# Performance work log

Hardware: AMD Instinct MI355X
Metric: run time of the kernel (lower is better)

## Reference

```python
import jax, jax.numpy as jnp
import numpy as np

E, H, V = 512, 1024, 50257
B, S = 64, 2048

def setup_inputs() -> dict:
    key = jax.random.key(0)
    ks = jax.random.split(key, 11)
    s_e, s_h, s_c, s_o = E ** -0.5, H ** -0.5, (2 * H) ** -0.5, H ** -0.5
    return {
        "input_seq_embedded": jax.random.normal(ks[0], (1, B, E), jnp.float32),
        "last_hidden": jax.random.normal(ks[1], (1, B, H), jnp.float32),
        "encoder_outputs": jax.random.normal(ks[2], (S, B, H), jnp.float32),
        # PyTorch GRU params (gate order: r, z, n)
        "w_ih": jax.random.uniform(ks[3], (3 * H, E), jnp.float32, -s_h, s_h),
        "w_hh": jax.random.uniform(ks[4], (3 * H, H), jnp.float32, -s_h, s_h),
        "b_ih": jax.random.uniform(ks[5], (3 * H,), jnp.float32, -s_h, s_h),
        "b_hh": jax.random.uniform(ks[6], (3 * H,), jnp.float32, -s_h, s_h),
        "W_concat": jax.random.uniform(ks[7], (H, 2 * H), jnp.float32, -s_c, s_c),
        "b_concat": jax.random.uniform(ks[8], (H,), jnp.float32, -s_c, s_c),
        "W_out": jax.random.uniform(ks[9], (V, H), jnp.float32, -s_o, s_o),
        "b_out": jax.random.uniform(ks[10], (V,), jnp.float32, -s_o, s_o),
    }

def reference(input_seq_embedded, last_hidden, encoder_outputs,
              w_ih, w_hh, b_ih, b_hh, W_concat, b_concat, W_out, b_out):
    x = input_seq_embedded[0]          # [B, E]
    h = last_hidden[0]                 # [B, H]
    # GRU cell (PyTorch semantics, gates r,z,n)
    gi = x @ w_ih.T + b_ih             # [B, 3H]
    gh = h @ w_hh.T + b_hh             # [B, 3H]
    gi_r, gi_z, gi_n = jnp.split(gi, 3, axis=1)
    gh_r, gh_z, gh_n = jnp.split(gh, 3, axis=1)
    r = jax.nn.sigmoid(gi_r + gh_r)
    z = jax.nn.sigmoid(gi_z + gh_z)
    n = jnp.tanh(gi_n + r * gh_n)
    h_new = (1.0 - z) * n + z * h      # [B, H]
    hidden = h_new[None]               # [1, B, H]
    rnn_output = h_new                 # [B, H] (seq dim squeezed)
    # 'dot' attention: energy[b,s] = <rnn_output[b], encoder_outputs[s,b]>
    energies = jnp.einsum('bh,sbh->bs', rnn_output, encoder_outputs)  # [B, S]
    attn_weights = jax.nn.softmax(energies, axis=1)                   # [B, S]
    context = jnp.einsum('bs,sbh->bh', attn_weights, encoder_outputs) # [B, H]
    concat_input = jnp.concatenate([rnn_output, context], axis=1)     # [B, 2H]
    concat_output = jnp.tanh(concat_input @ W_concat.T + b_concat)    # [B, H]
    output = concat_output @ W_out.T + b_out                          # [B, V]
    return output, hidden, attn_weights[:, None, :]
```

## Files before the change

### kernel.cpp

```cpp
#include <hip/hip_runtime.h>
#include <hip/hip_bf16.h>

#define E_DIM 512
#define H_DIM 1024
#define V_DIM 50257
#define B_DIM 64
#define S_DIM 2048

typedef unsigned short ushort_t;
typedef __attribute__((ext_vector_type(8))) short bf16x8;
typedef __attribute__((ext_vector_type(4))) float f32x4;

__device__ __forceinline__ ushort_t f2b(float f) {
    __hip_bfloat16 h = __float2bfloat16(f);
    ushort_t u;
    __builtin_memcpy(&u, &h, 2);
    return u;
}
__device__ __forceinline__ float dot4(float4 a, float4 b) {
    return a.x * b.x + a.y * b.y + a.z * b.z + a.w * b.w;
}

__global__ __launch_bounds__(256) void k_gru(
    const float* __restrict__ x,
    const float* __restrict__ h,
    const float* __restrict__ w_ih,
    const float* __restrict__ w_hh,
    const float* __restrict__ b_ih,
    const float* __restrict__ b_hh,
    float* __restrict__ ws_hnew,
    float* __restrict__ out_hidden)
{
    int g = blockIdx.x * 256 + threadIdx.x;
    int b = g & 63;
    int jh = g >> 6;
    const float4* x4 = (const float4*)(x + b * E_DIM);
    const float4* h4 = (const float4*)(h + b * H_DIM);
    const float4* wr_i = (const float4*)(w_ih + (size_t)jh * E_DIM);
    const float4* wz_i = (const float4*)(w_ih + (size_t)(jh + H_DIM) * E_DIM);
    const float4* wn_i = (const float4*)(w_ih + (size_t)(jh + 2 * H_DIM) * E_DIM);
    const float4* wr_h = (const float4*)(w_hh + (size_t)jh * H_DIM);
    const float4* wz_h = (const float4*)(w_hh + (size_t)(jh + H_DIM) * H_DIM);
    const float4* wn_h = (const float4*)(w_hh + (size_t)(jh + 2 * H_DIM) * H_DIM);

    float gir = 0.f, giz = 0.f, gin = 0.f;
    for (int e4 = 0; e4 < E_DIM / 4; ++e4) {
        float4 xv = x4[e4];
        gir += dot4(xv, wr_i[e4]);
        giz += dot4(xv, wz_i[e4]);
        gin += dot4(xv, wn_i[e4]);
    }
    float ghr = 0.f, ghz = 0.f, ghn = 0.f;
    for (int k4 = 0; k4 < H_DIM / 4; ++k4) {
        float4 hv = h4[k4];
        ghr += dot4(hv, wr_h[k4]);
        ghz += dot4(hv, wz_h[k4]);
        ghn += dot4(hv, wn_h[k4]);
    }
    gir += b_ih[jh];             ghr += b_hh[jh];
    giz += b_ih[jh + H_DIM];     ghz += b_hh[jh + H_DIM];
    gin += b_ih[jh + 2 * H_DIM]; ghn += b_hh[jh + 2 * H_DIM];

    float r = 1.f / (1.f + expf(-(gir + ghr)));
    float z = 1.f / (1.f + expf(-(giz + ghz)));
    float n = tanhf(gin + r * ghn);
    float hprev = h[b * H_DIM + jh];
    float hnew = (1.f - z) * n + z * hprev;
    ws_hnew[b * H_DIM + jh] = hnew;
    out_hidden[b * H_DIM + jh] = hnew;
}

__global__ __launch_bounds__(256) void k_energy(
    const float* __restrict__ enc,
    const float* __restrict__ hnew,
    float* __restrict__ energy)
{
    int wave = (blockIdx.x * 256 + threadIdx.x) >> 6;
    int lane = threadIdx.x & 63;
    int b = wave >> 8;
    int s8 = wave & 255;

    const float4* hv = (const float4*)(hnew + b * H_DIM + lane * 16);
    float4 h0 = hv[0], h1 = hv[1], h2 = hv[2], h3 = hv[3];

    for (int it = 0; it < 8; ++it) {
        int s = s8 * 8 + it;
        const float4* ev = (const float4*)(enc + ((size_t)s * B_DIM + b) * H_DIM + lane * 16);
        float acc = dot4(ev[0], h0) + dot4(ev[1], h1) + dot4(ev[2], h2) + dot4(ev[3], h3);
        #pragma unroll
        for (int off = 32; off; off >>= 1) acc += __shfl_xor(acc, off, 64);
        if (lane == 0) energy[b * S_DIM + s] = acc;
    }
}

__global__ __launch_bounds__(256) void k_softmax(
    float* __restrict__ energy,
    float* __restrict__ out_attn)
{
    int b = blockIdx.x, t = threadIdx.x;
    int lane = t & 63, wid = t >> 6;
    float e[8];
    #pragma unroll
    for (int i = 0; i < 8; ++i) e[i] = energy[b * S_DIM + i * 256 + t];
    float m = e[0];
    #pragma unroll
    for (int i = 1; i < 8; ++i) m = fmaxf(m, e[i]);
    #pragma unroll
    for (int off = 32; off; off >>= 1) m = fmaxf(m, __shfl_xor(m, off, 64));
    __shared__ float redm[4];
    __shared__ float reds[4];
    if (lane == 0) redm[wid] = m;
    __syncthreads();
    m = fmaxf(fmaxf(redm[0], redm[1]), fmaxf(redm[2], redm[3]));
    float p[8], ps = 0.f;
    #pragma unroll
    for (int i = 0; i < 8; ++i) { p[i] = expf(e[i] - m); ps += p[i]; }
    #pragma unroll
    for (int off = 32; off; off >>= 1) ps += __shfl_xor(ps, off, 64);
    if (lane == 0) reds[wid] = ps;
    __syncthreads();
    ps = reds[0] + reds[1] + reds[2] + reds[3];
    float inv = 1.f / ps;
    #pragma unroll
    for (int i = 0; i < 8; ++i) {
        float w = p[i] * inv;
        energy[b * S_DIM + i * 256 + t] = w;
        out_attn[b * S_DIM + i * 256 + t] = w;
    }
}

__global__ __launch_bounds__(256) void k_context(
    const float* __restrict__ enc,
    const float* __restrict__ wgt,
    float* __restrict__ ctxpart)
{
    int blk = blockIdx.x;
    int b = blk >> 4, c = blk & 15;
    int t = threadIdx.x;
    float4 a = {0.f, 0.f, 0.f, 0.f};
    for (int s = c * 128; s < c * 128 + 128; ++s) {
        float w = wgt[b * S_DIM + s];
        const float4* ev = (const float4*)(enc + ((size_t)s * B_DIM + b) * H_DIM);
        float4 v = ev[t];
        a.x += w * v.x; a.y += w * v.y; a.z += w * v.z; a.w += w * v.w;
    }
    ((float4*)(ctxpart + (size_t)(b * 16 + c) * H_DIM))[t] = a;
}

__global__ __launch_bounds__(256) void k_ctxsum(
    const float* __restrict__ ctxpart,
    float* __restrict__ ctx)
{
    int g = blockIdx.x * 256 + threadIdx.x;
    int b = g >> 10, hh = g & 1023;
    float acc = 0.f;
    #pragma unroll
    for (int c = 0; c < 16; ++c) acc += ctxpart[(size_t)(b * 16 + c) * H_DIM + hh];
    ctx[b * H_DIM + hh] = acc;
}

__global__ __launch_bounds__(256) void k_concat(
    const float* __restrict__ hnew, const float* __restrict__ ctx,
    const float* __restrict__ Wc,
    const float* __restrict__ bc,
    ushort_t* __restrict__ Xb)
{
    int g = blockIdx.x * 256 + threadIdx.x;
    int b = g & 63, jo = g >> 6;
    const float4* w1 = (const float4*)(Wc + (size_t)jo * 2 * H_DIM);
    const float4* w2 = (const float4*)(Wc + (size_t)jo * 2 * H_DIM + H_DIM);
    const float4* hv = (const float4*)(hnew + b * H_DIM);
    const float4* cv = (const float4*)(ctx + b * H_DIM);
    float acc = bc[jo];
    for (int k4 = 0; k4 < H_DIM / 4; ++k4) {
        acc += dot4(hv[k4], w1[k4]);
        acc += dot4(cv[k4], w2[k4]);
    }
    Xb[b * H_DIM + jo] = f2b(tanhf(acc));
}

__global__ __launch_bounds__(256) void k_out(
    const float* __restrict__ Wout,
    const ushort_t* __restrict__ Xb,
    const float* __restrict__ bout,
    float* __restrict__ out)
{
    int wave = (blockIdx.x * 256 + threadIdx.x) >> 6;
    int lane = threadIdx.x & 63;
    int v0 = wave * 16;
    if (v0 >= V_DIM) return;
    int m = lane & 15, quad = lane >> 4;
    int arow = v0 + m;
    if (arow > V_DIM - 1) arow = V_DIM - 1;
    const float* wr = Wout + (size_t)arow * H_DIM + quad * 8;
    const short* xrow = (const short*)Xb + m * H_DIM + quad * 8;

    f32x4 acc[4] = {{0.f, 0.f, 0.f, 0.f}, {0.f, 0.f, 0.f, 0.f},
                    {0.f, 0.f, 0.f, 0.f}, {0.f, 0.f, 0.f, 0.f}};
    for (int k0 = 0; k0 < H_DIM; k0 += 32) {
        float4 a0 = *(const float4*)(wr + k0);
        float4 a1 = *(const float4*)(wr + k0 + 4);
        bf16x8 a;
        a[0] = (short)f2b(a0.x); a[1] = (short)f2b(a0.y);
        a[2] = (short)f2b(a0.z); a[3] = (short)f2b(a0.w);
        a[4] = (short)f2b(a1.x); a[5] = (short)f2b(a1.y);
        a[6] = (short)f2b(a1.z); a[7] = (short)f2b(a1.w);
        #pragma unroll
        for (int bt = 0; bt < 4; ++bt) {
            bf16x8 bb = *(const bf16x8*)(xrow + bt * 16 * H_DIM + k0);
            acc[bt] = __builtin_amdgcn_mfma_f32_16x16x32_bf16(a, bb, acc[bt], 0, 0, 0);
        }
    }
    #pragma unroll
    for (int bt = 0; bt < 4; ++bt) {
        int b = bt * 16 + m;
        #pragma unroll
        for (int r = 0; r < 4; ++r) {
            int v = v0 + quad * 4 + r;
            if (v < V_DIM) out[(size_t)b * V_DIM + v] = acc[bt][r] + bout[v];
        }
    }
}

extern "C" void kernel_launch(void* const* d_in, const int* in_sizes, int n_in,
                              void* d_out, int out_size, void* d_ws, size_t ws_size,
                              hipStream_t stream) {
    const float* x    = (const float*)d_in[0];
    const float* h    = (const float*)d_in[1];
    const float* enc  = (const float*)d_in[2];
    const float* w_ih = (const float*)d_in[3];
    const float* w_hh = (const float*)d_in[4];
    const float* b_ih = (const float*)d_in[5];
    const float* b_hh = (const float*)d_in[6];
    const float* Wc   = (const float*)d_in[7];
    const float* bc   = (const float*)d_in[8];
    const float* Wout = (const float*)d_in[9];
    const float* bout = (const float*)d_in[10];

    float* out        = (float*)d_out;
    float* out_hidden = out + (size_t)B_DIM * V_DIM;
    float* out_attn   = out_hidden + B_DIM * H_DIM;

    char* ws = (char*)d_ws;
    float* ws_hnew    = (float*)ws;
    float* ws_energy  = (float*)(ws + (256 << 10));
    float* ws_ctx     = (float*)(ws + (768 << 10));
    ushort_t* ws_Xb   = (ushort_t*)(ws + (1024 << 10));
    float* ws_ctxpart = (float*)(ws + (1152 << 10));

    k_gru<<<B_DIM * H_DIM / 256, 256, 0, stream>>>(x, h, w_ih, w_hh, b_ih, b_hh,
                                                   ws_hnew, out_hidden);
    k_energy<<<B_DIM * S_DIM / 8 / 4, 256, 0, stream>>>(enc, ws_hnew, ws_energy);
    k_softmax<<<B_DIM, 256, 0, stream>>>(ws_energy, out_attn);
    k_context<<<B_DIM * 16, 256, 0, stream>>>(enc, ws_energy, ws_ctxpart);
    k_ctxsum<<<B_DIM * H_DIM / 256, 256, 0, stream>>>(ws_ctxpart, ws_ctx);
    k_concat<<<B_DIM * H_DIM / 256, 256, 0, stream>>>(ws_hnew, ws_ctx, Wc, bc, ws_Xb);
    int waves4 = (V_DIM + 15) / 16;
    k_out<<<(waves4 + 3) / 4, 256, 0, stream>>>(Wout, ws_Xb, bout, out);
}
```

Measured before the change: 1.173 ms.

## Fuse energy, softmax and context into one online-softmax pass over encoder outputs

Replaces the separate energy, softmax, context and context-sum kernels with a single flash-style kernel that computes energies and accumulates the weighted context using an online max/sum rescale. A small finish kernel merges per-chunk partials and writes normalized attention weights. This removes the second full read of the large encoder tensor and several launches. It adds serial rescaling work per wave and uses fast exp approximations.

```diff
diff --git a/kernel.cpp b/kernel.cpp
--- a/kernel.cpp
+++ b/kernel.cpp
@@ -70,97 +70,137 @@
     out_hidden[b * H_DIM + jh] = hnew;
 }
 
-__global__ __launch_bounds__(256) void k_energy(
+__global__ __launch_bounds__(256) void k_attn(
     const float* __restrict__ enc,
     const float* __restrict__ hnew,
-    float* __restrict__ energy)
-{
-    int wave = (blockIdx.x * 256 + threadIdx.x) >> 6;
+    float* __restrict__ e_out,
+    float* __restrict__ mpart,
+    float* __restrict__ lpart,
+    float* __restrict__ ctxpart)
+{
+    int b = blockIdx.x >> 4;
+    int c = blockIdx.x & 15;
+    int w = threadIdx.x >> 6;
     int lane = threadIdx.x & 63;
-    int b = wave >> 8;
-    int s8 = wave & 255;
+    int s0 = c * 128 + w * 32;
 
     const float4* hv = (const float4*)(hnew + b * H_DIM + lane * 16);
     float4 h0 = hv[0], h1 = hv[1], h2 = hv[2], h3 = hv[3];
 
-    for (int it = 0; it < 8; ++it) {
-        int s = s8 * 8 + it;
-        const float4* ev = (const float4*)(enc + ((size_t)s * B_DIM + b) * H_DIM + lane * 16);
-        float acc = dot4(ev[0], h0) + dot4(ev[1], h1) + dot4(ev[2], h2) + dot4(ev[3], h3);
-        #pragma unroll
-        for (int off = 32; off; off >>= 1) acc += __shfl_xor(acc, off, 64);
-        if (lane == 0) energy[b * S_DIM + s] = acc;
-    }
-}
-
-__global__ __launch_bounds__(256) void k_softmax(
-    float* __restrict__ energy,
+    const size_t sstride = (size_t)B_DIM * H_DIM;
+    const float* p = enc + ((size_t)s0 * B_DIM + b) * H_DIM + lane * 16;
+
+    float4 a0 = {0.f, 0.f, 0.f, 0.f}, a1 = a0, a2 = a0, a3 = a0;
+    float m = -3.0e38f, l = 0.f;
+
+    float4 v0 = ((const float4*)p)[0];
+    float4 v1 = ((const float4*)p)[1];
+    float4 v2 = ((const float4*)p)[2];
+    float4 v3 = ((const float4*)p)[3];
+
+    for (int it = 0; it < 32; ++it) {
+        float4 n0, n1, n2, n3;
+        const float* pn = p + sstride;
+        if (it < 31) {
+            n0 = ((const float4*)pn)[0];
+            n1 = ((const float4*)pn)[1];
+            n2 = ((const float4*)pn)[2];
+            n3 = ((const float4*)pn)[3];
+        }
+        float e = dot4(v0, h0) + dot4(v1, h1) + dot4(v2, h2) + dot4(v3, h3);
+        #pragma unroll
+        for (int off = 32; off; off >>= 1) e += __shfl_xor(e, off, 64);
+        if (lane == 0) e_out[b * S_DIM + s0 + it] = e;
+        if (e > m) {
+            float sc = __expf(m - e);
+            l *= sc;
+            a0.x *= sc; a0.y *= sc; a0.z *= sc; a0.w *= sc;
+            a1.x *= sc; a1.y *= sc; a1.z *= sc; a1.w *= sc;
+            a2.x *= sc; a2.y *= sc; a2.z *= sc; a2.w *= sc;
+            a3.x *= sc; a3.y *= sc; a3.z *= sc; a3.w *= sc;
+            m = e;
+        }
+        float pw = __expf(e - m);
+        l += pw;
+        a0.x += pw * v0.x; a0.y += pw * v0.y; a0.z += pw * v0.z; a0.w += pw * v0.w;
+        a1.x += pw * v1.x; a1.y += pw * v1.y; a1.z += pw * v1.z; a1.w += pw * v1.w;
+        a2.x += pw * v2.x; a2.y += pw * v2.y; a2.z += pw * v2.z; a2.w += pw * v2.w;
+        a3.x += pw * v3.x; a3.y += pw * v3.y; a3.z += pw * v3.z; a3.w += pw * v3.w;
+        if (it < 31) {
+            p = pn;
+            v0 = n0; v1 = n1; v2 = n2; v3 = n3;
+        }
+    }
+
+    __shared__ float sa[4][H_DIM];
+    __shared__ float sml[8];
+    float* dst = &sa[w][lane * 16];
+    ((float4*)dst)[0] = a0; ((float4*)dst)[1] = a1;
+    ((float4*)dst)[2] = a2; ((float4*)dst)[3] = a3;
+    if (lane == 0) { sml[w] = m; sml[4 + w] = l; }
+    __syncthreads();
+
+    float M = fmaxf(fmaxf(sml[0], sml[1]), fmaxf(sml[2], sml[3]));
+    float sc0 = __expf(sml[0] - M), sc1 = __expf(sml[1] - M);
+    float sc2 = __expf(sml[2] - M), sc3 = __expf(sml[3] - M);
+    int t = threadIdx.x;
+    float4 r0 = ((const float4*)&sa[0][0])[t];
+    float4 r1 = ((const float4*)&sa[1][0])[t];
+    float4 r2 = ((const float4*)&sa[2][0])[t];
+    float4 r3 = ((const float4*)&sa[3][0])[t];
+    float4 r;
+    r.x = sc0 * r0.x + sc1 * r1.x + sc2 * r2.x + sc3 * r3.x;
+    r.y = sc0 * r0.y + sc1 * r1.y + sc2 * r2.y + sc3 * r3.y;
+    r.z = sc0 * r0.z + sc1 * r1.z + sc2 * r2.z + sc3 * r3.z;
+    r.w = sc0 * r0.w + sc1 * r1.w + sc2 * r2.w + sc3 * r3.w;
+    ((float4*)(ctxpart + (size_t)(b * 16 + c) * H_DIM))[t] = r;
+    if (t == 0) {
+        float Lc = sc0 * sml[4] + sc1 * sml[5] + sc2 * sml[6] + sc3 * sml[7];
+        mpart[b * 16 + c] = M;
+        lpart[b * 16 + c] = Lc;
+    }
+}
+
+__global__ __launch_bounds__(256) void k_finish(
+    const float* __restrict__ e_in,
+    const float* __restrict__ mpart,
+    const float* __restrict__ lpart,
+    float* ctxpart,
     float* __restrict__ out_attn)
 {
-    int b = blockIdx.x, t = threadIdx.x;
-    int lane = t & 63, wid = t >> 6;
-    float e[8];
+    int b = blockIdx.x >> 2, q = blockIdx.x & 3;
+    int t = threadIdx.x, lane = t & 63, wid = t >> 6;
+    __shared__ float sSc[16];
+    __shared__ float sM, sInvL;
+    if (wid == 0) {
+        float mc = (lane < 16) ? mpart[b * 16 + lane] : -3.0e38f;
+        float lc = (lane < 16) ? lpart[b * 16 + lane] : 0.f;
+        float M = mc;
+        #pragma unroll
+        for (int off = 32; off; off >>= 1) M = fmaxf(M, __shfl_xor(M, off, 64));
+        float sc = (lane < 16) ? __expf(mc - M) : 0.f;
+        if (lane < 16) sSc[lane] = sc;
+        float L = lc * sc;
+        #pragma unroll
+        for (int off = 32; off; off >>= 1) L += __shfl_xor(L, off, 64);
+        if (lane == 0) { sM = M; sInvL = 1.f / L; }
+    }
+    __syncthreads();
+    float M = sM, invL = sInvL;
+    float* cp = ctxpart + (size_t)b * 16 * H_DIM + q * 256 + t;
+    float a = 0.f;
     #pragma unroll
-    for (int i = 0; i < 8; ++i) e[i] = energy[b * S_DIM + i * 256 + t];
-    float m = e[0];
-    #pragma unroll
-    for (int i = 1; i < 8; ++i) m = fmaxf(m, e[i]);
-    #pragma unroll
-    for (int off = 32; off; off >>= 1) m = fmaxf(m, __shfl_xor(m, off, 64));
-    __shared__ float redm[4];
-    __shared__ float reds[4];
-    if (lane == 0) redm[wid] = m;
-    __syncthreads();
-    m = fmaxf(fmaxf(redm[0], redm[1]), fmaxf(redm[2], redm[3]));
-    float p[8], ps = 0.f;
-    #pragma unroll
-    for (int i = 0; i < 8; ++i) { p[i] = expf(e[i] - m); ps += p[i]; }
-    #pragma unroll
-    for (int off = 32; off; off >>= 1) ps += __shfl_xor(ps, off, 64);
-    if (lane == 0) reds[wid] = ps;
-    __syncthreads();
-    ps = reds[0] + reds[1] + reds[2] + reds[3];
-    float inv = 1.f / ps;
-    #pragma unroll
-    for (int i = 0; i < 8; ++i) {
-        float w = p[i] * inv;
-        energy[b * S_DIM + i * 256 + t] = w;
-        out_attn[b * S_DIM + i * 256 + t] = w;
-    }
-}
-
-__global__ __launch_bounds__(256) void k_context(
-    const float* __restrict__ enc,
-    const float* __restrict__ wgt,
-    float* __restrict__ ctxpart)
-{
-    int blk = blockIdx.x;
-    int b = blk >> 4, c = blk & 15;
-    int t = threadIdx.x;
-    float4 a = {0.f, 0.f, 0.f, 0.f};
-    for (int s = c * 128; s < c * 128 + 128; ++s) {
-        float w = wgt[b * S_DIM + s];
-        const float4* ev = (const float4*)(enc + ((size_t)s * B_DIM + b) * H_DIM);
-        float4 v = ev[t];
-        a.x += w * v.x; a.y += w * v.y; a.z += w * v.z; a.w += w * v.w;
-    }
-    ((float4*)(ctxpart + (size_t)(b * 16 + c) * H_DIM))[t] = a;
-}
-
-__global__ __launch_bounds__(256) void k_ctxsum(
-    const float* __restrict__ ctxpart,
-    float* __restrict__ ctx)
-{
-    int g = blockIdx.x * 256 + threadIdx.x;
-    int b = g >> 10, hh = g & 1023;
-    float acc = 0.f;
-    #pragma unroll
-    for (int c = 0; c < 16; ++c) acc += ctxpart[(size_t)(b * 16 + c) * H_DIM + hh];
-    ctx[b * H_DIM + hh] = acc;
+    for (int c0 = 0; c0 < 16; ++c0) a += sSc[c0] * cp[(size_t)c0 * H_DIM];
+    cp[0] = a * invL;
+    const float* eb = e_in + b * S_DIM + q * 512;
+    float* ab = out_attn + b * S_DIM + q * 512;
+    ab[t]       = __expf(eb[t]       - M) * invL;
+    ab[t + 256] = __expf(eb[t + 256] - M) * invL;
 }
 
 __global__ __launch_bounds__(256) void k_concat(
-    const float* __restrict__ hnew, const float* __restrict__ ctx,
+    const float* __restrict__ hnew,
+    const float* __restrict__ ctx16,
     const float* __restrict__ Wc,
     const float* __restrict__ bc,
     ushort_t* __restrict__ Xb)
@@ -170,7 +210,7 @@
     const float4* w1 = (const float4*)(Wc + (size_t)jo * 2 * H_DIM);
     const float4* w2 = (const float4*)(Wc + (size_t)jo * 2 * H_DIM + H_DIM);
     const float4* hv = (const float4*)(hnew + b * H_DIM);
-    const float4* cv = (const float4*)(ctx + b * H_DIM);
+    const float4* cv = (const float4*)(ctx16 + (size_t)b * 16 * H_DIM);
     float acc = bc[jo];
     for (int k4 = 0; k4 < H_DIM / 4; ++k4) {
         acc += dot4(hv[k4], w1[k4]);
@@ -243,18 +283,19 @@
 
     char* ws = (char*)d_ws;
     float* ws_hnew    = (float*)ws;
-    float* ws_energy  = (float*)(ws + (256 << 10));
-    float* ws_ctx     = (float*)(ws + (768 << 10));
-    ushort_t* ws_Xb   = (ushort_t*)(ws + (1024 << 10));
-    float* ws_ctxpart = (float*)(ws + (1152 << 10));
+    float* ws_e       = (float*)(ws + (256 << 10));
+    float* ws_m       = (float*)(ws + (768 << 10));
+    float* ws_l       = (float*)(ws + (772 << 10));
+    ushort_t* ws_Xb   = (ushort_t*)(ws + (776 << 10));
+    float* ws_ctxpart = (float*)(ws + (904 << 10));
 
     k_gru<<<B_DIM * H_DIM / 256, 256, 0, stream>>>(x, h, w_ih, w_hh, b_ih, b_hh,
                                                    ws_hnew, out_hidden);
-    k_energy<<<B_DIM * S_DIM / 8 / 4, 256, 0, stream>>>(enc, ws_hnew, ws_energy);
-    k_softmax<<<B_DIM, 256, 0, stream>>>(ws_energy, out_attn);
-    k_context<<<B_DIM * 16, 256, 0, stream>>>(enc, ws_energy, ws_ctxpart);
-    k_ctxsum<<<B_DIM * H_DIM / 256, 256, 0, stream>>>(ws_ctxpart, ws_ctx);
-    k_concat<<<B_DIM * H_DIM / 256, 256, 0, stream>>>(ws_hnew, ws_ctx, Wc, bc, ws_Xb);
+    k_attn<<<B_DIM * 16, 256, 0, stream>>>(enc, ws_hnew, ws_e, ws_m, ws_l,
+                                           ws_ctxpart);
+    k_finish<<<B_DIM * 4, 256, 0, stream>>>(ws_e, ws_m, ws_l, ws_ctxpart, out_attn);
+    k_concat<<<B_DIM * H_DIM / 256, 256, 0, stream>>>(ws_hnew, ws_ctxpart, Wc, bc,
+                                                      ws_Xb);
     int waves4 = (V_DIM + 15) / 16;
     k_out<<<(waves4 + 3) / 4, 256, 0, stream>>>(Wout, ws_Xb, bout, out);
 }
```

Result: faster. 1.088 ms (-7.2%).
